# Optimization experiments

Measured on AMD Instinct MI355X. Metric: run time of the kernel, lower is better.

Reference implementation:

```python
import jax, jax.numpy as jnp
import numpy as np

B, H, W, D, C = 1, 32, 32, 32, 512
NH, P = 8, 8
HD = C // NH          # head dim = 64
N = P ** 3            # tokens per window = 512
HID = 4 * C           # mlp hidden = 2048
EPS = 1e-5            # torch LayerNorm default


def setup_inputs() -> dict:
    key = jax.random.key(0)
    ks = jax.random.split(key, 8)
    init = lambda k, shape, fan: jax.random.normal(k, shape, jnp.float32) / np.sqrt(fan).astype(np.float32)
    return {
        "x": jax.random.normal(ks[0], (B, H, W, D, C), jnp.float32),
        "q_ms": jax.random.normal(ks[1], (B, NH, N, HD), jnp.float32),
        "norm1_w": jnp.ones((C,), jnp.float32),
        "norm1_b": jnp.zeros((C,), jnp.float32),
        "kv_w": init(ks[2], (C, 2 * C), C),
        "kv_b": jnp.zeros((2 * C,), jnp.float32),
        "proj_w": init(ks[3], (C, C), C),
        "proj_b": jnp.zeros((C,), jnp.float32),
        "norm2_w": jnp.ones((C,), jnp.float32),
        "norm2_b": jnp.zeros((C,), jnp.float32),
        "fc1_w": init(ks[4], (C, HID), C),
        "fc1_b": jnp.zeros((HID,), jnp.float32),
        "fc2_w": init(ks[5], (HID, C), HID),
        "fc2_b": jnp.zeros((C,), jnp.float32),
    }


def layernorm(x, w, b):
    m = jnp.mean(x, axis=-1, keepdims=True)
    v = jnp.mean(jnp.square(x - m), axis=-1, keepdims=True)
    return (x - m) * jax.lax.rsqrt(v + EPS) * w + b


def reference(x, q_ms, norm1_w, norm1_b, kv_w, kv_b, proj_w, proj_b,
              norm2_w, norm2_b, fc1_w, fc1_b, fc2_w, fc2_b):
    shortcut = x
    xn = layernorm(x, norm1_w, norm1_b)
    # get_patches: (B,H,W,D,C) -> (B*nw, N, C), windows in (nh,nw,nd) order
    xw = xn.reshape(B, H // P, P, W // P, P, D // P, P, C)
    xw = xw.transpose(0, 1, 3, 5, 2, 4, 6, 7).reshape(-1, N, C)
    Bw = xw.shape[0]  # B * num_windows = 64
    # global attention: kv from window tokens, shared multi-scale query q_ms
    kv = (xw @ kv_w + kv_b).reshape(Bw, N, 2, NH, HD).transpose(2, 0, 3, 1, 4)
    k, v = kv[0], kv[1]  # (Bw, NH, N, HD)
    scale = HD ** -0.5
    q = jnp.tile(q_ms, (Bw // B, 1, 1, 1)) * scale  # replicate query across windows
    attn = jax.nn.softmax(jnp.einsum('bhqd,bhkd->bhqk', q, k), axis=-1)
    o = jnp.einsum('bhqk,bhkd->bhqd', attn, v)
    o = o.transpose(0, 2, 1, 3).reshape(Bw, N, C)
    o = o @ proj_w + proj_b
    # get_image: (B*nw, N, C) -> (B,H,W,D,C)
    xi = o.reshape(B, H // P, W // P, D // P, P, P, P, C)
    xi = xi.transpose(0, 1, 4, 2, 5, 3, 6, 7).reshape(B, H, W, D, C)
    x1 = shortcut + xi
    h = layernorm(x1, norm2_w, norm2_b)
    h = jax.nn.gelu(h @ fc1_w + fc1_b, approximate=False) @ fc2_w + fc2_b
    return x1 + h
```

## Files before the change

### kernel.cpp

```cpp
#include <hip/hip_runtime.h>

typedef unsigned short u16;
typedef __attribute__((ext_vector_type(8))) short bfrag;
typedef __attribute__((ext_vector_type(4))) float ffrag;

#define LN_EPS 1e-5f

#define GLOAD16(g, l)                                                          \
    __builtin_amdgcn_global_load_lds(                                          \
        (const __attribute__((address_space(1))) void*)(g),                    \
        (__attribute__((address_space(3))) void*)(l), 16, 0, 0)

__device__ __forceinline__ u16 f2bf(float f) {
    unsigned u = __builtin_bit_cast(unsigned, f);
    u += 0x7fffu + ((u >> 16) & 1u);
    return (u16)(u >> 16);
}

__device__ __forceinline__ float bf2f(u16 b) {
    unsigned u = ((unsigned)b) << 16;
    return __builtin_bit_cast(float, u);
}

__device__ __forceinline__ int win_to_img(int tok) {
    int win = tok >> 9, n = tok & 511;
    int wh = win >> 4, ww = (win >> 2) & 3, wd = win & 3;
    int ph = n >> 6, pw = (n >> 3) & 7, pd = n & 7;
    return ((wh * 8 + ph) * 32 + (ww * 8 + pw)) * 32 + (wd * 8 + pd);
}

__global__ __launch_bounds__(256) void k_ln(const float* __restrict__ x,
                                            const float* __restrict__ w,
                                            const float* __restrict__ b,
                                            u16* __restrict__ out, int windowed) {
    int wave = threadIdx.x >> 6, lane = threadIdx.x & 63;
    int tok = blockIdx.x * 4 + wave;
    int src = windowed ? win_to_img(tok) : tok;
    const float* xr = x + (size_t)src * 512;
    float v[8];
#pragma unroll
    for (int i = 0; i < 2; i++) {
        float4 f = *(const float4*)(xr + i * 256 + lane * 4);
        v[i * 4 + 0] = f.x; v[i * 4 + 1] = f.y; v[i * 4 + 2] = f.z; v[i * 4 + 3] = f.w;
    }
    float s = 0.f;
#pragma unroll
    for (int i = 0; i < 8; i++) s += v[i];
#pragma unroll
    for (int m = 1; m < 64; m <<= 1) s += __shfl_xor(s, m);
    float mean = s * (1.0f / 512.0f);
    float vs = 0.f;
#pragma unroll
    for (int i = 0; i < 8; i++) { float d = v[i] - mean; vs += d * d; }
#pragma unroll
    for (int m = 1; m < 64; m <<= 1) vs += __shfl_xor(vs, m);
    float rstd = rsqrtf(vs * (1.0f / 512.0f) + LN_EPS);
    u16* orow = out + (size_t)tok * 512;
#pragma unroll
    for (int i = 0; i < 2; i++) {
        int c0 = i * 256 + lane * 4;
        ushort4 o;
        o.x = f2bf((v[i * 4 + 0] - mean) * rstd * w[c0 + 0] + b[c0 + 0]);
        o.y = f2bf((v[i * 4 + 1] - mean) * rstd * w[c0 + 1] + b[c0 + 1]);
        o.z = f2bf((v[i * 4 + 2] - mean) * rstd * w[c0 + 2] + b[c0 + 2]);
        o.w = f2bf((v[i * 4 + 3] - mean) * rstd * w[c0 + 3] + b[c0 + 3]);
        *(ushort4*)(orow + c0) = o;
    }
}

__global__ __launch_bounds__(256) void k_lnb(const u16* __restrict__ x,
                                             const float* __restrict__ w,
                                             const float* __restrict__ b,
                                             u16* __restrict__ out) {
    int wave = threadIdx.x >> 6, lane = threadIdx.x & 63;
    int tok = blockIdx.x * 4 + wave;
    const u16* xr = x + (size_t)tok * 512 + lane * 8;
    bfrag raw = *(const bfrag*)(xr);
    float v[8];
#pragma unroll
    for (int i = 0; i < 8; i++) v[i] = bf2f((u16)raw[i]);
    float s = 0.f;
#pragma unroll
    for (int i = 0; i < 8; i++) s += v[i];
#pragma unroll
    for (int m = 1; m < 64; m <<= 1) s += __shfl_xor(s, m);
    float mean = s * (1.0f / 512.0f);
    float vs = 0.f;
#pragma unroll
    for (int i = 0; i < 8; i++) { float d = v[i] - mean; vs += d * d; }
#pragma unroll
    for (int m = 1; m < 64; m <<= 1) vs += __shfl_xor(vs, m);
    float rstd = rsqrtf(vs * (1.0f / 512.0f) + LN_EPS);
    int c0 = lane * 8;
    ushort4 o0, o1;
    o0.x = f2bf((v[0] - mean) * rstd * w[c0 + 0] + b[c0 + 0]);
    o0.y = f2bf((v[1] - mean) * rstd * w[c0 + 1] + b[c0 + 1]);
    o0.z = f2bf((v[2] - mean) * rstd * w[c0 + 2] + b[c0 + 2]);
    o0.w = f2bf((v[3] - mean) * rstd * w[c0 + 3] + b[c0 + 3]);
    o1.x = f2bf((v[4] - mean) * rstd * w[c0 + 4] + b[c0 + 4]);
    o1.y = f2bf((v[5] - mean) * rstd * w[c0 + 5] + b[c0 + 5]);
    o1.z = f2bf((v[6] - mean) * rstd * w[c0 + 6] + b[c0 + 6]);
    o1.w = f2bf((v[7] - mean) * rstd * w[c0 + 7] + b[c0 + 7]);
    u16* orow = out + (size_t)tok * 512 + c0;
    *(ushort4*)(orow) = o0;
    *(ushort4*)(orow + 4) = o1;
}

__global__ __launch_bounds__(256) void k_prep(const float* __restrict__ kv_w,
                                              const float* __restrict__ proj_w,
                                              const float* __restrict__ fc1_w,
                                              const float* __restrict__ fc2_w,
                                              const float* __restrict__ q,
                                              u16* __restrict__ kv_wt,
                                              u16* __restrict__ proj_wt,
                                              u16* __restrict__ fc1_wt,
                                              u16* __restrict__ fc2_wt,
                                              u16* __restrict__ qbf) {
    int i = blockIdx.x * 256 + threadIdx.x;
    if (i < 524288) {
        int n = i >> 9, k = i & 511;
        kv_wt[i] = f2bf(kv_w[k * 1024 + n]);
    } else if (i < 786432) {
        int j = i - 524288, n = j >> 9, k = j & 511;
        proj_wt[j] = f2bf(proj_w[k * 512 + n]);
    } else if (i < 1835008) {
        int j = i - 786432, n = j >> 9, k = j & 511;
        fc1_wt[j] = f2bf(fc1_w[k * 2048 + n]);
    } else if (i < 2883584) {
        int j = i - 1835008, n = j >> 11, k = j & 2047;
        fc2_wt[j] = f2bf(fc2_w[k * 512 + n]);
    } else {
        int j = i - 2883584;
        qbf[j] = f2bf(q[j] * 0.125f);
    }
}

template <int EPI>
__global__ __launch_bounds__(256, 4) void k_gemm128(const u16* __restrict__ A,
                                                    const u16* __restrict__ Bt,
                                                    const float* __restrict__ bias,
                                                    void* __restrict__ Cout, int K, int Nn,
                                                    const float* __restrict__ resid,
                                                    void* __restrict__ Cout2) {
    __shared__ u16 As0[4096], Bs0[4096], As1[4096], Bs1[4096];
    int tid = threadIdx.x;
    int wave = tid >> 6, lane = tid & 63;
    int wr = wave >> 1, wc = wave & 1;

    int gx = Nn >> 7;
    int nwg = gridDim.x;
    int wg = blockIdx.x;
    int wgs = (wg & 7) * (nwg >> 3) + (wg >> 3);
    int bn = wgs % gx, bm = wgs / gx;

    int rt = wave * 32 + (lane >> 2);
    int sxo = ((lane & 3) ^ ((rt ^ (rt >> 2)) & 3)) * 8;
    const u16* Ag = A + (size_t)(bm * 128 + rt) * K + sxo;
    const u16* Bg = Bt + (size_t)(bn * 128 + rt) * K + sxo;

    int fr = lane & 15, g = lane >> 4;
    int pco = (g ^ ((fr ^ (fr >> 2)) & 3)) * 8;

    ffrag acc[4][4] = {};

#define STAGE(AS, BS, k0)                                                      \
    {                                                                          \
        GLOAD16(Ag + (k0), AS + wave * 1024);                                  \
        GLOAD16(Ag + (k0) + 16 * K, AS + wave * 1024 + 512);                   \
        GLOAD16(Bg + (k0), BS + wave * 1024);                                  \
        GLOAD16(Bg + (k0) + 16 * K, BS + wave * 1024 + 512);                   \
    }
#define COMPUTE(AS, BS)                                                        \
    {                                                                          \
        bfrag a[4], b[4];                                                      \
        _Pragma("unroll") for (int m = 0; m < 4; m++)                          \
            a[m] = *(const bfrag*)(AS + (wr * 64 + m * 16 + fr) * 32 + pco);   \
        _Pragma("unroll") for (int n = 0; n < 4; n++)                          \
            b[n] = *(const bfrag*)(BS + (wc * 64 + n * 16 + fr) * 32 + pco);   \
        _Pragma("unroll") for (int m = 0; m < 4; m++)                          \
            _Pragma("unroll") for (int n = 0; n < 4; n++)                      \
                acc[m][n] = __builtin_amdgcn_mfma_f32_16x16x32_bf16(           \
                    a[m], b[n], acc[m][n], 0, 0, 0);                           \
    }

    int nt = K >> 5;
    STAGE(As0, Bs0, 0);
    __syncthreads();
    int t = 0;
    for (; t + 2 < nt; t += 2) {
        STAGE(As1, Bs1, (t + 1) * 32);
        COMPUTE(As0, Bs0);
        __syncthreads();
        STAGE(As0, Bs0, (t + 2) * 32);
        COMPUTE(As1, Bs1);
        __syncthreads();
    }
    STAGE(As1, Bs1, (nt - 1) * 32);
    COMPUTE(As0, Bs0);
    __syncthreads();
    COMPUTE(As1, Bs1);
#undef STAGE
#undef COMPUTE

    int gcolb = bn * 128 + wc * 64;
    int grb = bm * 128 + wr * 64;

    __syncthreads();
    u16* ep = (wave == 0) ? As0 : (wave == 1) ? Bs0 : (wave == 2) ? As1 : Bs1;

    if constexpr (EPI == 0) {
        int h = (gcolb >> 6) & 7;
        bool isK = (gcolb < 512);
#pragma unroll
        for (int m = 0; m < 4; m++)
#pragma unroll
            for (int n = 0; n < 4; n++) {
                float bv = bias[gcolb + n * 16 + fr];
#pragma unroll
                for (int r = 0; r < 4; r++) {
                    int wq = m * 16 + g * 4 + r;
                    int wcc = n * 16 + fr;
                    float val = acc[m][n][r] + bv;
                    if (isK)
                        ep[wq * 64 + (wcc ^ ((wq & 7) << 3))] = f2bf(val);
                    else
                        ep[wcc * 64 + (wq ^ ((wcc & 7) << 3))] = f2bf(val);
                }
            }
#pragma unroll
        for (int rd = 0; rd < 8; rd++) {
            int row = rd * 8 + (lane >> 3);
            int ch = (lane & 7) ^ (row & 7);
            int4 v = *(const int4*)(ep + row * 64 + ch * 8);
            if (isK) {
                int tok = grb + row;
                int win = tok >> 9, key = tok & 511;
                *(int4*)(&((u16*)Cout)[(((size_t)(win * 8 + h)) * 512 + key) * 64 + (lane & 7) * 8]) = v;
            } else {
                int win = grb >> 9, key0 = grb & 511;
                *(int4*)(&((u16*)Cout2)[(((size_t)(win * 8 + h)) * 64 + row) * 512 + key0 + (lane & 7) * 8]) = v;
            }
        }
    } else {
#pragma unroll
        for (int m = 0; m < 4; m++)
#pragma unroll
            for (int n = 0; n < 4; n++) {
                float bv = bias[gcolb + n * 16 + fr];
#pragma unroll
                for (int r = 0; r < 4; r++) {
                    int wq = m * 16 + g * 4 + r;
                    int ri = win_to_img(grb + wq);
                    float val = acc[m][n][r] + bv +
                                resid[(size_t)ri * 512 + gcolb + n * 16 + fr];
                    int wcc = n * 16 + fr;
                    ep[wq * 64 + (wcc ^ ((wq & 7) << 3))] = f2bf(val);
                }
            }
#pragma unroll
        for (int rd = 0; rd < 8; rd++) {
            int row = rd * 8 + (lane >> 3);
            int ch = (lane & 7) ^ (row & 7);
            int4 v = *(const int4*)(ep + row * 64 + ch * 8);
            int ri = win_to_img(grb + row);
            *(int4*)(&((u16*)Cout)[(size_t)ri * 512 + gcolb + (lane & 7) * 8]) = v;
        }
    }
}

template <int EPI>
__global__ __launch_bounds__(512, 2) void k_gemm256p(const u16* __restrict__ A,
                                                     const u16* __restrict__ Bt,
                                                     const float* __restrict__ bias,
                                                     void* __restrict__ Cout, int K, int Nn,
                                                     const void* __restrict__ resid) {
    __shared__ u16 sm[65536];
    int tid = threadIdx.x;
    int wave = tid >> 6, lane = tid & 63;
    int wm = wave >> 2, wn = wave & 3;

    int gx = Nn >> 8;
    int nwg = gridDim.x;
    int wg = blockIdx.x;
    int wgs = (wg & 7) * (nwg >> 3) + (wg >> 3);
    int bn = wgs % gx, bm = wgs / gx;

    int sr = tid >> 3;
    int sf = (sr ^ (sr >> 2)) & 7;
    int sxo = ((tid & 7) ^ sf) * 8;
    const u16* Ag = A + (size_t)(bm * 256 + sr) * K + sxo;
    const u16* Bg = Bt + (size_t)(bn * 256 + sr) * K + sxo;
    size_t rowK = (size_t)64 * K;

    int fr = lane & 15, g = lane >> 4;
    int fb0 = (fr ^ (fr >> 2)) & 7;

    ffrag acc[8][4] = {};

#define STAGE256(SLOT, k0)                                                     \
    {                                                                          \
        u16* d = sm + (SLOT) * 32768 + wave * 512;                             \
        _Pragma("unroll") for (int i = 0; i < 4; i++)                          \
            GLOAD16(Ag + (k0) + i * rowK, d + i * 4096);                       \
        _Pragma("unroll") for (int i = 0; i < 4; i++)                          \
            GLOAD16(Bg + (k0) + i * rowK, d + 16384 + i * 4096);               \
    }

    int nt = K >> 6;
    STAGE256(0, 0);
    asm volatile("s_waitcnt vmcnt(0)" ::: "memory");
    __builtin_amdgcn_sched_barrier(0);
    __builtin_amdgcn_s_barrier();
    __builtin_amdgcn_sched_barrier(0);

#pragma unroll 1
    for (int t = 0; t < nt; ++t) {
        const u16* Ab = sm + (t & 1) * 32768;
        const u16* Bb = Ab + 16384;
        if (t + 1 < nt) STAGE256((t + 1) & 1, (size_t)(t + 1) * 64);
        bfrag bfr[8];
#pragma unroll
        for (int n = 0; n < 4; n++)
#pragma unroll
            for (int s = 0; s < 2; s++)
                bfr[n * 2 + s] = *(const bfrag*)(Bb + (wn * 64 + n * 16 + fr) * 64 +
                                  (((g + 4 * s) ^ fb0 ^ ((n & 1) << 2)) & 7) * 8);
#pragma unroll
        for (int q = 0; q < 4; q++) {
            bfrag afr[4];
#pragma unroll
            for (int mm = 0; mm < 2; mm++)
#pragma unroll
                for (int s = 0; s < 2; s++) {
                    int m = q * 2 + mm;
                    afr[mm * 2 + s] = *(const bfrag*)(Ab + (wm * 128 + m * 16 + fr) * 64 +
                                      (((g + 4 * s) ^ fb0 ^ ((m & 1) << 2)) & 7) * 8);
                }
            __builtin_amdgcn_s_setprio(1);
#pragma unroll
            for (int mm = 0; mm < 2; mm++)
#pragma unroll
                for (int n = 0; n < 4; n++)
#pragma unroll
                    for (int s = 0; s < 2; s++)
                        acc[q * 2 + mm][n] = __builtin_amdgcn_mfma_f32_16x16x32_bf16(
                            afr[mm * 2 + s], bfr[n * 2 + s], acc[q * 2 + mm][n], 0, 0, 0);
            __builtin_amdgcn_s_setprio(0);
        }
        asm volatile("s_waitcnt lgkmcnt(0)" ::: "memory");
        asm volatile("s_waitcnt vmcnt(0)" ::: "memory");
        __builtin_amdgcn_sched_barrier(0);
        __builtin_amdgcn_s_barrier();
        __builtin_amdgcn_sched_barrier(0);
    }
#undef STAGE256

    int gcb = bn * 256 + wn * 64;
    int grb = bm * 256 + wm * 128;

    if constexpr (EPI == 2) {
        u16* ep = sm + wave * 8192;
#pragma unroll
        for (int m = 0; m < 8; m++)
#pragma unroll
            for (int n = 0; n < 4; n++) {
                float bv = bias[gcb + n * 16 + fr];
#pragma unroll
                for (int r = 0; r < 4; r++) {
                    int rl = m * 16 + g * 4 + r;
                    int cl = n * 16 + fr;
                    float xx = acc[m][n][r] + bv;
                    float inner = fmaf(0.044715f * xx * xx, xx, xx);
                    float e = __expf(-1.5957691216f * inner);
                    float val = xx * __builtin_amdgcn_rcpf(1.0f + e);
                    ep[rl * 64 + (cl ^ ((rl & 7) << 3))] = f2bf(val);
                }
            }
#pragma unroll
        for (int it = 0; it < 16; it++) {
            int rl = it * 8 + (lane >> 3);
            int ch = (lane & 7) ^ (rl & 7);
            int4 v = *(const int4*)(ep + rl * 64 + ch * 8);
            *(int4*)(&((u16*)Cout)[(size_t)(grb + rl) * Nn + gcb + (lane & 7) * 8]) = v;
        }
    } else {
        const u16* rb = (const u16*)resid;
#pragma unroll
        for (int m = 0; m < 8; m++)
#pragma unroll
            for (int n = 0; n < 4; n++) {
                int col = gcb + n * 16 + fr;
                float bv = bias[col];
#pragma unroll
                for (int r = 0; r < 4; r++) {
                    int row = grb + m * 16 + g * 4 + r;
                    size_t o = (size_t)row * 512 + col;
                    ((float*)Cout)[o] = acc[m][n][r] + bv + bf2f(rb[o]);
                }
            }
    }
}

__global__ __launch_bounds__(256, 4) void k_attn(const u16* __restrict__ qb,
                                                 const u16* __restrict__ kb,
                                                 const u16* __restrict__ vtb,
                                                 u16* __restrict__ o) {
    __shared__ u16 K0[4096], K1[4096], V0[4096], V1[4096];
    __shared__ u16 Ps[4096];
    int bid = blockIdx.x;
    int wg = (bid & 7) * 512 + (bid >> 3);
    int qc = wg & 7;
    int pair = wg >> 3;
    int hh = pair & 7, win = pair >> 3;
    int wave = threadIdx.x >> 6, lane = threadIdx.x & 63;
    const u16* kbw = kb + ((size_t)(win * 8 + hh)) * 512 * 64;
    const u16* vtw = vtb + ((size_t)(win * 8 + hh)) * 64 * 512;

    const u16* qrow = qb + ((size_t)hh * 512 + qc * 64 + (wave << 4) + (lane & 15)) * 64 + (lane >> 4) * 8;
    bfrag aq0 = *(const bfrag*)(qrow);
    bfrag aq1 = *(const bfrag*)(qrow + 32);

    ffrag acc[4] = {};
    float m_run[4], l_run[4];
#pragma unroll
    for (int r = 0; r < 4; r++) { m_run[r] = -1e30f; l_run[r] = 0.0f; }

    int srow = lane >> 3;
    int sxo = ((lane & 7) ^ srow) * 8;
    int fr = lane & 15;
    int fkc = lane >> 4;
    int kx0 = (fkc ^ (fr & 7)) * 8;
    int kx1 = ((fkc + 4) ^ (fr & 7)) * 8;
    int arow = (wave << 4) + fr;
    int pswz = (arow & 7) << 3;

#define STAGE_KV(KS, VS, kc)                                                   \
    {                                                                          \
        GLOAD16(kbw + (size_t)((kc) * 64 + wave * 8 + srow) * 64 + sxo,        \
                KS + wave * 512);                                              \
        GLOAD16(kbw + (size_t)((kc) * 64 + 32 + wave * 8 + srow) * 64 + sxo,   \
                KS + 2048 + wave * 512);                                       \
        GLOAD16(vtw + (size_t)(wave * 8 + srow) * 512 + (kc) * 64 + sxo,       \
                VS + wave * 512);                                              \
        GLOAD16(vtw + (size_t)(32 + wave * 8 + srow) * 512 + (kc) * 64 + sxo,  \
                VS + 2048 + wave * 512);                                       \
    }
#define ATT_COMPUTE(KS, VS)                                                    \
    {                                                                          \
        ffrag s[4] = {};                                                       \
        _Pragma("unroll") for (int j = 0; j < 4; j++) {                        \
            bfrag b0 = *(const bfrag*)(KS + (j * 16 + fr) * 64 + kx0);         \
            s[j] = __builtin_amdgcn_mfma_f32_16x16x32_bf16(aq0, b0, s[j], 0, 0, 0); \
            bfrag b1 = *(const bfrag*)(KS + (j * 16 + fr) * 64 + kx1);         \
            s[j] = __builtin_amdgcn_mfma_f32_16x16x32_bf16(aq1, b1, s[j], 0, 0, 0); \
        }                                                                      \
        int need = 0;                                                          \
        _Pragma("unroll") for (int r = 0; r < 4; r++) {                        \
            float mxj = fmaxf(fmaxf(s[0][r], s[1][r]),                         \
                              fmaxf(s[2][r], s[3][r]));                        \
            need |= (mxj > m_run[r] + 8.0f) ? 1 : 0;                           \
        }                                                                      \
        if (__any(need)) {                                                     \
            _Pragma("unroll") for (int r = 0; r < 4; r++) {                    \
                float mx = fmaxf(fmaxf(s[0][r], s[1][r]),                      \
                                 fmaxf(s[2][r], s[3][r]));                     \
                _Pragma("unroll") for (int d = 1; d < 16; d <<= 1)             \
                    mx = fmaxf(mx, __shfl_xor(mx, d));                         \
                float mnew = fmaxf(m_run[r], mx);                              \
                float alpha = __expf(m_run[r] - mnew);                         \
                m_run[r] = mnew;                                               \
                l_run[r] *= alpha;                                             \
                _Pragma("unroll") for (int j = 0; j < 4; j++)                  \
                    acc[j][r] *= alpha;                                        \
            }                                                                  \
        }                                                                      \
        _Pragma("unroll") for (int j = 0; j < 4; j++)                          \
            _Pragma("unroll") for (int r = 0; r < 4; r++) {                    \
                float p = __expf(s[j][r] - m_run[r]);                          \
                l_run[r] += p;                                                 \
                int prow = (wave << 4) + (lane >> 4) * 4 + r;                  \
                Ps[prow * 64 + ((j * 16 + fr) ^ ((prow & 7) << 3))] = f2bf(p); \
            }                                                                  \
        bfrag ap0 = *(const bfrag*)(&Ps[arow * 64 + ((fkc * 8) ^ pswz)]);      \
        bfrag ap1 = *(const bfrag*)(&Ps[arow * 64 + ((32 + fkc * 8) ^ pswz)]); \
        _Pragma("unroll") for (int j = 0; j < 4; j++) {                        \
            bfrag v0 = *(const bfrag*)(VS + (j * 16 + fr) * 64 + kx0);         \
            acc[j] = __builtin_amdgcn_mfma_f32_16x16x32_bf16(ap0, v0, acc[j], 0, 0, 0); \
            bfrag v1 = *(const bfrag*)(VS + (j * 16 + fr) * 64 + kx1);         \
            acc[j] = __builtin_amdgcn_mfma_f32_16x16x32_bf16(ap1, v1, acc[j], 0, 0, 0); \
        }                                                                      \
    }

    STAGE_KV(K0, V0, 0);
    __syncthreads();
#pragma unroll 1
    for (int kc = 0; kc < 8; kc += 2) {
        if (kc + 1 < 8) STAGE_KV(K1, V1, kc + 1);
        ATT_COMPUTE(K0, V0);
        __syncthreads();
        if (kc + 2 < 8) STAGE_KV(K0, V0, kc + 2);
        ATT_COMPUTE(K1, V1);
        __syncthreads();
    }
#undef STAGE_KV
#undef ATT_COMPUTE

#pragma unroll
    for (int r = 0; r < 4; r++) {
#pragma unroll
        for (int d = 1; d < 16; d <<= 1)
            l_run[r] += __shfl_xor(l_run[r], d);
    }

    int row0 = qc * 64 + (wave << 4) + (lane >> 4) * 4;
#pragma unroll
    for (int j = 0; j < 4; j++) {
        int col = hh * 64 + j * 16 + fr;
#pragma unroll
        for (int r = 0; r < 4; r++) {
            float val = acc[j][r] / l_run[r];
            o[((size_t)win * 512 + row0 + r) * 512 + col] = f2bf(val);
        }
    }
}

extern "C" void kernel_launch(void* const* d_in, const int* in_sizes, int n_in,
                              void* d_out, int out_size, void* d_ws, size_t ws_size,
                              hipStream_t stream) {
    const float* x      = (const float*)d_in[0];
    const float* q_ms   = (const float*)d_in[1];
    const float* n1w    = (const float*)d_in[2];
    const float* n1b    = (const float*)d_in[3];
    const float* kv_w   = (const float*)d_in[4];
    const float* kv_b   = (const float*)d_in[5];
    const float* proj_w = (const float*)d_in[6];
    const float* proj_b = (const float*)d_in[7];
    const float* n2w    = (const float*)d_in[8];
    const float* n2b    = (const float*)d_in[9];
    const float* fc1_w  = (const float*)d_in[10];
    const float* fc1_b  = (const float*)d_in[11];
    const float* fc2_w  = (const float*)d_in[12];
    const float* fc2_b  = (const float*)d_in[13];

    char* ws = (char*)d_ws;
    const size_t OFF_XNW = 0;
    const size_t OFF_KB  = 33554432;
    const size_t OFF_VT  = 67108864;
    const size_t OFF_O   = 100663296;
    const size_t OFF_HID = 0;
    const size_t OFF_X1  = 134217728;
    const size_t OFF_XN2 = 201326592;
    const size_t OFF_W   = 234881024;
    u16* xnw = (u16*)(ws + OFF_XNW);
    u16* kbb = (u16*)(ws + OFF_KB);
    u16* vtb = (u16*)(ws + OFF_VT);
    u16* ob  = (u16*)(ws + OFF_O);
    u16* hid = (u16*)(ws + OFF_HID);
    u16* x1b = (u16*)(ws + OFF_X1);
    u16* xn2 = (u16*)(ws + OFF_XN2);
    u16* kv_wt   = (u16*)(ws + OFF_W);
    u16* proj_wt = kv_wt + 512 * 1024;
    u16* fc1_wt  = proj_wt + 512 * 512;
    u16* fc2_wt  = fc1_wt + 512 * 2048;
    u16* qbf     = fc2_wt + 2048 * 512;
    size_t need = OFF_W + (size_t)(512 * 1024 + 512 * 512 + 512 * 2048 + 2048 * 512 + 8 * 512 * 64) * 2;
    if (ws_size < need) return;

    k_ln<<<8192, 256, 0, stream>>>(x, n1w, n1b, xnw, 1);
    k_prep<<<12288, 256, 0, stream>>>(kv_w, proj_w, fc1_w, fc2_w, q_ms,
                                      kv_wt, proj_wt, fc1_wt, fc2_wt, qbf);

    k_gemm128<0><<<2048, 256, 0, stream>>>(xnw, kv_wt, kv_b, kbb, 512, 1024, nullptr, vtb);
    k_attn<<<dim3(4096), 256, 0, stream>>>(qbf, kbb, vtb, ob);
    k_gemm128<1><<<1024, 256, 0, stream>>>(ob, proj_wt, proj_b, x1b, 512, 512, x, nullptr);
    k_lnb<<<8192, 256, 0, stream>>>(x1b, n2w, n2b, xn2);
    k_gemm256p<2><<<1024, 512, 0, stream>>>(xn2, fc1_wt, fc1_b, hid, 512, 2048, nullptr);
    k_gemm256p<3><<<256, 512, 0, stream>>>(hid, fc2_wt, fc2_b, d_out, 2048, 512, x1b);
}
```

Measured before the change: 376.7 us.

## Triple-buffer 256x256 GEMM with K=32 stages to cut LDS footprint

```diff
diff --git a/kernel.cpp b/kernel.cpp
--- a/kernel.cpp
+++ b/kernel.cpp
@@ -274,7 +274,7 @@
                                                      const float* __restrict__ bias,
                                                      void* __restrict__ Cout, int K, int Nn,
                                                      const void* __restrict__ resid) {
-    __shared__ u16 sm[65536];
+    __shared__ u16 sm[49152];
     int tid = threadIdx.x;
     int wave = tid >> 6, lane = tid & 63;
     int wm = wave >> 2, wn = wave & 3;
@@ -285,103 +285,104 @@
     int wgs = (wg & 7) * (nwg >> 3) + (wg >> 3);
     int bn = wgs % gx, bm = wgs / gx;
 
-    int sr = tid >> 3;
-    int sf = (sr ^ (sr >> 2)) & 7;
-    int sxo = ((tid & 7) ^ sf) * 8;
-    const u16* Ag = A + (size_t)(bm * 256 + sr) * K + sxo;
-    const u16* Bg = Bt + (size_t)(bn * 256 + sr) * K + sxo;
-    size_t rowK = (size_t)64 * K;
+    int rt = tid >> 2;
+    int sxo = ((tid & 3) ^ ((rt ^ (rt >> 2)) & 3)) * 8;
+    const u16* Ag = A + (size_t)(bm * 256 + rt) * K + sxo;
+    const u16* Bg = Bt + (size_t)(bn * 256 + rt) * K + sxo;
+    size_t half = (size_t)128 * K;
+    int wl = wave * 512;
 
     int fr = lane & 15, g = lane >> 4;
-    int fb0 = (fr ^ (fr >> 2)) & 7;
+    int pco = (g ^ ((fr ^ (fr >> 2)) & 3)) * 8;
 
     ffrag acc[8][4] = {};
 
-#define STAGE256(SLOT, k0)                                                     \
+#define STAGE3(SLOT, k0)                                                       \
     {                                                                          \
-        u16* d = sm + (SLOT) * 32768 + wave * 512;                             \
-        _Pragma("unroll") for (int i = 0; i < 4; i++)                          \
-            GLOAD16(Ag + (k0) + i * rowK, d + i * 4096);                       \
-        _Pragma("unroll") for (int i = 0; i < 4; i++)                          \
-            GLOAD16(Bg + (k0) + i * rowK, d + 16384 + i * 4096);               \
-    }
-
-    int nt = K >> 6;
-    STAGE256(0, 0);
-    asm volatile("s_waitcnt vmcnt(0)" ::: "memory");
+        u16* d = sm + (SLOT) * 16384 + wl;                                     \
+        GLOAD16(Ag + (k0), d);                                                 \
+        GLOAD16(Ag + (k0) + half, d + 4096);                                   \
+        GLOAD16(Bg + (k0), d + 8192);                                          \
+        GLOAD16(Bg + (k0) + half, d + 12288);                                  \
+    }
+#define COMPUTE3(SLOT)                                                         \
+    {                                                                          \
+        const u16* Ab = sm + (SLOT) * 16384;                                   \
+        const u16* Bb = Ab + 8192;                                             \
+        bfrag a[8], b[4];                                                      \
+        _Pragma("unroll") for (int m = 0; m < 8; m++)                          \
+            a[m] = *(const bfrag*)(Ab + (wm * 128 + m * 16 + fr) * 32 + pco);  \
+        _Pragma("unroll") for (int n = 0; n < 4; n++)                          \
+            b[n] = *(const bfrag*)(Bb + (wn * 64 + n * 16 + fr) * 32 + pco);   \
+        __builtin_amdgcn_s_setprio(1);                                         \
+        _Pragma("unroll") for (int m = 0; m < 8; m++)                          \
+            _Pragma("unroll") for (int n = 0; n < 4; n++)                      \
+                acc[m][n] = __builtin_amdgcn_mfma_f32_16x16x32_bf16(           \
+                    a[m], b[n], acc[m][n], 0, 0, 0);                           \
+        __builtin_amdgcn_s_setprio(0);                                         \
+    }
+#define PHASE3(tt, SLOT)                                                       \
+    if ((tt) < nt) {                                                           \
+        if ((tt) + 2 < nt) STAGE3(((tt) + 2) % 3, ((tt) + 2) * 32);            \
+        COMPUTE3(SLOT);                                                        \
+        asm volatile("s_waitcnt lgkmcnt(0)" ::: "memory");                     \
+        if ((tt) + 2 < nt) {                                                   \
+            asm volatile("s_waitcnt vmcnt(4)" ::: "memory");                   \
+        } else if ((tt) + 1 < nt) {                                            \
+            asm volatile("s_waitcnt vmcnt(0)" ::: "memory");                   \
+        }                                                                      \
+        __builtin_amdgcn_sched_barrier(0);                                     \
+        __builtin_amdgcn_s_barrier();                                          \
+        __builtin_amdgcn_sched_barrier(0);                                     \
+    }
+
+    int nt = K >> 5;
+    STAGE3(0, 0);
+    STAGE3(1, 32);
+    asm volatile("s_waitcnt vmcnt(4)" ::: "memory");
     __builtin_amdgcn_sched_barrier(0);
     __builtin_amdgcn_s_barrier();
     __builtin_amdgcn_sched_barrier(0);
-
 #pragma unroll 1
-    for (int t = 0; t < nt; ++t) {
-        const u16* Ab = sm + (t & 1) * 32768;
-        const u16* Bb = Ab + 16384;
-        if (t + 1 < nt) STAGE256((t + 1) & 1, (size_t)(t + 1) * 64);
-        bfrag bfr[8];
-#pragma unroll
-        for (int n = 0; n < 4; n++)
-#pragma unroll
-            for (int s = 0; s < 2; s++)
-                bfr[n * 2 + s] = *(const bfrag*)(Bb + (wn * 64 + n * 16 + fr) * 64 +
-                                  (((g + 4 * s) ^ fb0 ^ ((n & 1) << 2)) & 7) * 8);
-#pragma unroll
-        for (int q = 0; q < 4; q++) {
-            bfrag afr[4];
-#pragma unroll
-            for (int mm = 0; mm < 2; mm++)
-#pragma unroll
-                for (int s = 0; s < 2; s++) {
-                    int m = q * 2 + mm;
-                    afr[mm * 2 + s] = *(const bfrag*)(Ab + (wm * 128 + m * 16 + fr) * 64 +
-                                      (((g + 4 * s) ^ fb0 ^ ((m & 1) << 2)) & 7) * 8);
-                }
-            __builtin_amdgcn_s_setprio(1);
-#pragma unroll
-            for (int mm = 0; mm < 2; mm++)
-#pragma unroll
-                for (int n = 0; n < 4; n++)
-#pragma unroll
-                    for (int s = 0; s < 2; s++)
-                        acc[q * 2 + mm][n] = __builtin_amdgcn_mfma_f32_16x16x32_bf16(
-                            afr[mm * 2 + s], bfr[n * 2 + s], acc[q * 2 + mm][n], 0, 0, 0);
-            __builtin_amdgcn_s_setprio(0);
-        }
-        asm volatile("s_waitcnt lgkmcnt(0)" ::: "memory");
-        asm volatile("s_waitcnt vmcnt(0)" ::: "memory");
-        __builtin_amdgcn_sched_barrier(0);
-        __builtin_amdgcn_s_barrier();
-        __builtin_amdgcn_sched_barrier(0);
-    }
-#undef STAGE256
+    for (int t = 0; t < nt; t += 3) {
+        PHASE3(t, 0);
+        PHASE3(t + 1, 1);
+        PHASE3(t + 2, 2);
+    }
+#undef STAGE3
+#undef COMPUTE3
+#undef PHASE3
 
     int gcb = bn * 256 + wn * 64;
     int grb = bm * 256 + wm * 128;
 
     if constexpr (EPI == 2) {
-        u16* ep = sm + wave * 8192;
-#pragma unroll
-        for (int m = 0; m < 8; m++)
-#pragma unroll
-            for (int n = 0; n < 4; n++) {
-                float bv = bias[gcb + n * 16 + fr];
-#pragma unroll
-                for (int r = 0; r < 4; r++) {
-                    int rl = m * 16 + g * 4 + r;
-                    int cl = n * 16 + fr;
-                    float xx = acc[m][n][r] + bv;
-                    float inner = fmaf(0.044715f * xx * xx, xx, xx);
-                    float e = __expf(-1.5957691216f * inner);
-                    float val = xx * __builtin_amdgcn_rcpf(1.0f + e);
-                    ep[rl * 64 + (cl ^ ((rl & 7) << 3))] = f2bf(val);
+        u16* ep = sm + wave * 4096;
+#pragma unroll
+        for (int p = 0; p < 2; p++) {
+#pragma unroll
+            for (int m = 0; m < 4; m++)
+#pragma unroll
+                for (int n = 0; n < 4; n++) {
+                    float bv = bias[gcb + n * 16 + fr];
+#pragma unroll
+                    for (int r = 0; r < 4; r++) {
+                        int rl = m * 16 + g * 4 + r;
+                        int cl = n * 16 + fr;
+                        float xx = acc[p * 4 + m][n][r] + bv;
+                        float inner = fmaf(0.044715f * xx * xx, xx, xx);
+                        float e = __expf(-1.5957691216f * inner);
+                        float val = xx * __builtin_amdgcn_rcpf(1.0f + e);
+                        ep[rl * 64 + (cl ^ ((rl & 7) << 3))] = f2bf(val);
+                    }
                 }
+#pragma unroll
+            for (int it = 0; it < 8; it++) {
+                int rl = it * 8 + (lane >> 3);
+                int ch = (lane & 7) ^ (rl & 7);
+                int4 v = *(const int4*)(ep + rl * 64 + ch * 8);
+                *(int4*)(&((u16*)Cout)[(size_t)(grb + p * 64 + rl) * Nn + gcb + (lane & 7) * 8]) = v;
             }
-#pragma unroll
-        for (int it = 0; it < 16; it++) {
-            int rl = it * 8 + (lane >> 3);
-            int ch = (lane & 7) ^ (rl & 7);
-            int4 v = *(const int4*)(ep + rl * 64 + ch * 8);
-            *(int4*)(&((u16*)Cout)[(size_t)(grb + rl) * Nn + gcb + (lane & 7) * 8]) = v;
         }
     } else {
         const u16* rb = (const u16*)resid;
```

New measurement: 389.2 us. 1.03x slower.
